# Kernel tuning notes

Hardware: AMD Instinct MI355X
Metric: run time of the kernel (lower is better)

Reference implementation:

```python
import jax, jax.numpy as jnp
import numpy as np

B, N, D = 2, 2048, 512
H, HD = 8, 64
R = 64  # graph_radius
SCALE = HD ** -0.5
LN_EPS = 1e-5


def _ln(x, g, b):
    m = jnp.mean(x, axis=-1, keepdims=True)
    v = jnp.mean((x - m) ** 2, axis=-1, keepdims=True)
    return (x - m) * jax.lax.rsqrt(v + LN_EPS) * g + b


def setup_inputs() -> dict:
    key = jax.random.key(0)
    ks = jax.random.split(key, 8)
    w = lambda k, shape: (jax.random.normal(k, shape, jnp.float32) * 0.02)
    return {
        "nodes": jax.random.normal(ks[0], (B, N, D), jnp.float32),
        "ln1_g": jnp.ones((D,), jnp.float32), "ln1_b": jnp.zeros((D,), jnp.float32),
        "qkv_w": w(ks[1], (D, 3 * D)), "qkv_b": jnp.zeros((3 * D,), jnp.float32),
        "proj_w": w(ks[2], (D, D)), "proj_b": jnp.zeros((D,), jnp.float32),
        "rep_scale": jnp.ones((H,), jnp.float32),
        "rel_bias": w(ks[3], (2 * N - 1, H)),
        "ln2_g": jnp.ones((D,), jnp.float32), "ln2_b": jnp.zeros((D,), jnp.float32),
        "mlp_w1": w(ks[4], (D, 2 * D)), "mlp_b1": jnp.zeros((2 * D,), jnp.float32),
        "mlp_w2": w(ks[5], (2 * D, D)), "mlp_b2": jnp.zeros((D,), jnp.float32),
    }


def reference(nodes, ln1_g, ln1_b, qkv_w, qkv_b, proj_w, proj_b, rep_scale,
              rel_bias, ln2_g, ln2_b, mlp_w1, mlp_b1, mlp_w2, mlp_b2):
    b, n, d = nodes.shape
    x = _ln(nodes, ln1_g, ln1_b)                       # [B,N,D]
    qkv = (x @ qkv_w + qkv_b).reshape(b, n, 3, H, HD)
    qkv = jnp.transpose(qkv, (2, 0, 3, 1, 4))          # [3,B,H,N,HD]
    q, k, v = qkv[0], qkv[1], qkv[2]
    logits = jnp.einsum('bhnd,bhmd->bhnm', q, k) * SCALE
    # representation correlation (F.normalize with eps=1e-12)
    rep = x / jnp.maximum(jnp.linalg.norm(x, axis=-1, keepdims=True), 1e-12)
    corr = jnp.einsum('bnd,bmd->bnm', rep, rep)        # [B,N,N]
    logits = logits + corr[:, None] * rep_scale[None, :, None, None]
    pos = jnp.arange(n)
    relidx = pos[:, None] - pos[None, :]               # [N,N]
    bias = rel_bias[relidx + n - 1]                    # [N,N,H]
    logits = logits + jnp.transpose(bias, (2, 0, 1))[None]
    mask = jnp.abs(relidx) <= R
    logits = jnp.where(mask[None, None], logits, -jnp.inf)
    attn = jax.nn.softmax(logits, axis=-1)
    upd = jnp.einsum('bhnm,bhmd->bnhd', attn, v).reshape(b, n, d)
    nodes = nodes + (upd @ proj_w + proj_b)
    y = _ln(nodes, ln2_g, ln2_b)
    h = jax.nn.gelu(y @ mlp_w1 + mlp_b1, approximate=False)
    return nodes + (h @ mlp_w2 + mlp_b2)
```

## Files before the change

### kernel.cpp

```cpp
#include <hip/hip_runtime.h>
#include <math.h>

typedef __bf16 bf16;
typedef __bf16 bf16x4 __attribute__((ext_vector_type(4)));
typedef __bf16 bf16x8 __attribute__((ext_vector_type(8)));
typedef float floatx4 __attribute__((ext_vector_type(4)));

#define BB 2
#define NN 2048
#define DD 512
#define HH 8
#define HD 64
#define RR 64
#define D3 1536
#define NEG_BIG (-1e30f)
#define TQ 32
#define TBAND 160

#define GL2LDS16(g, l)                                                        \
    __builtin_amdgcn_global_load_lds(                                         \
        (const __attribute__((address_space(1))) void*)(const void*)(g),      \
        (__attribute__((address_space(3))) void*)(void*)(l), 16, 0, 0)

static __device__ __forceinline__ float block_reduce_sum256(float v, float* sbuf) {
    const int tid = threadIdx.x;
    #pragma unroll
    for (int o = 32; o > 0; o >>= 1) v += __shfl_xor(v, o, 64);
    __syncthreads();
    if ((tid & 63) == 0) sbuf[tid >> 6] = v;
    __syncthreads();
    return sbuf[0] + sbuf[1] + sbuf[2] + sbuf[3];
}

static __device__ __forceinline__ void ln_row(
    float* sbuf, const float* in, const float* gw, const float* bw,
    bf16* out, float* invnorm, int row, bool want_inv) {
    const int tid = threadIdx.x;
    const int i0 = tid * 2;
    const float* ip = in + (size_t)row * DD;
    float v0 = ip[i0], v1 = ip[i0 + 1];
    float mean = block_reduce_sum256(v0 + v1, sbuf) * (1.f / DD);
    float d0 = v0 - mean, d1 = v1 - mean;
    float var = block_reduce_sum256(d0 * d0 + d1 * d1, sbuf) * (1.f / DD);
    float rs = rsqrtf(var + 1e-5f);
    float x0 = d0 * rs * gw[i0] + bw[i0];
    float x1 = d1 * rs * gw[i0 + 1] + bw[i0 + 1];
    out[(size_t)row * DD + i0] = (bf16)x0;
    out[(size_t)row * DD + i0 + 1] = (bf16)x1;
    if (want_inv) {
        float s2 = block_reduce_sum256(x0 * x0 + x1 * x1, sbuf);
        if (tid == 0) invnorm[row] = 1.f / fmaxf(sqrtf(s2), 1e-12f);
    }
}

union SMemCL {
    bf16 Ts[64][72];
    float sbuf[4];
};
__global__ __launch_bounds__(256) void cvt_ln_kernel(
    const float* __restrict__ qkv_w, const float* __restrict__ proj_w,
    const float* __restrict__ m1w, const float* __restrict__ m2w,
    bf16* __restrict__ wqt, bf16* __restrict__ wpt,
    bf16* __restrict__ w1t, bf16* __restrict__ w2t,
    const float* __restrict__ nodes, const float* __restrict__ ln1_g,
    const float* __restrict__ ln1_b, bf16* __restrict__ x,
    float* __restrict__ invn) {
    __shared__ SMemCL sm;
    const int tid = threadIdx.x;
    int bid = blockIdx.x;
    if (bid >= 512) {
        int r0 = (bid - 512) * 8;
        for (int r = 0; r < 8; r++)
            ln_row(sm.sbuf, nodes, ln1_g, ln1_b, x, invn, r0 + r, true);
        return;
    }
    const float* W; bf16* Wt; int K, N, bx, by;
    if (bid < 192)      { W = qkv_w; Wt = wqt; K = 512;  N = 1536; bx = bid % 24; by = bid / 24; }
    else if (bid < 256) { bid -= 192; W = proj_w; Wt = wpt; K = 512;  N = 512;  bx = bid % 8;  by = bid / 8; }
    else if (bid < 384) { bid -= 256; W = m1w; Wt = w1t; K = 512;  N = 1024; bx = bid % 16; by = bid / 16; }
    else                { bid -= 384; W = m2w; Wt = w2t; K = 1024; N = 512;  bx = bid % 8;  by = bid / 8; }
    const int n0 = bx * 64, k0 = by * 64;
    #pragma unroll
    for (int i = 0; i < 4; i++) {
        int r = (tid >> 4) + i * 16;
        int c = (tid & 15) * 4;
        floatx4 v = *(const floatx4*)(W + (size_t)(k0 + r) * N + n0 + c);
        #pragma unroll
        for (int e = 0; e < 4; e++) sm.Ts[r][c + e] = (bf16)v[e];
    }
    __syncthreads();
    #pragma unroll
    for (int i = 0; i < 4; i++) {
        int n = (tid >> 4) + i * 16;
        int k = (tid & 15) * 4;
        bf16x4 o;
        #pragma unroll
        for (int e = 0; e < 4; e++) o[e] = sm.Ts[k + e][n];
        *(bf16x4*)(Wt + (size_t)(n0 + n) * K + k0 + k) = o;
    }
}

union SMemQC {
    struct { bf16 As[2][4096], Bs[2][4096]; } g;
    struct { bf16 Ts[64][72]; } t;
    struct { bf16 Xc[TBAND * 72]; float invb[TBAND]; } c;
};
__global__ __launch_bounds__(256) void qkv_corr_kernel(
    const bf16* __restrict__ x, const bf16* __restrict__ wqt,
    const float* __restrict__ qkv_b, const float* __restrict__ invn,
    bf16* __restrict__ qkvb, bf16* __restrict__ vt_g,
    float* __restrict__ corr_g) {
    __shared__ SMemQC sm;
    const int tid = threadIdx.x;
    const int bid = blockIdx.x;
    const int w = tid >> 6, lane = tid & 63;
    const int lr = lane & 15, lq = lane >> 4;

    if (bid >= 1536) {
        const int item = bid - 1536;
        const int b = item & 1, n0 = (item >> 1) * TQ;
        const int bN = b * NN;
        const int rowHalf = (w >> 1) * 16, colBase = (w & 1) * 80;
        if (tid < TBAND) {
            int mc = min(max(n0 - RR + tid, 0), NN - 1);
            sm.c.invb[tid] = invn[bN + mc];
        }
        floatx4 cacc[5];
        #pragma unroll
        for (int t = 0; t < 5; t++) cacc[t] = (floatx4){0.f, 0.f, 0.f, 0.f};
        for (int c = 0; c < 8; c++) {
            __syncthreads();
            #pragma unroll
            for (int rr = 0; rr < 6; rr++) {
                int G = rr * 256 + tid;
                if (G < 1440) {
                    int j = G / 9, gc = G % 9;
                    int gcs = min(gc, 7);
                    int mc = min(max(n0 - RR + j, 0), NN - 1);
                    GL2LDS16(x + (size_t)(bN + mc) * DD + c * 64 + gcs * 8, sm.c.Xc + G * 8);
                }
            }
            __syncthreads();
            #pragma unroll
            for (int kb = 0; kb < 2; kb++) {
                bf16x8 a = *(bf16x8*)&sm.c.Xc[(64 + rowHalf + lr) * 72 + kb * 32 + lq * 8];
                #pragma unroll
                for (int t = 0; t < 5; t++) {
                    bf16x8 bb = *(bf16x8*)&sm.c.Xc[(colBase + t * 16 + lr) * 72 + kb * 32 + lq * 8];
                    cacc[t] = __builtin_amdgcn_mfma_f32_16x16x32_bf16(a, bb, cacc[t], 0, 0, 0);
                }
            }
        }
        float invq[4];
        #pragma unroll
        for (int r = 0; r < 4; r++) invq[r] = sm.c.invb[64 + rowHalf + lq * 4 + r];
        const size_t cbase = (size_t)item * TQ * TBAND;
        #pragma unroll
        for (int t = 0; t < 5; t++) {
            float invk = sm.c.invb[colBase + t * 16 + lr];
            #pragma unroll
            for (int r = 0; r < 4; r++)
                corr_g[cbase + (size_t)(rowHalf + lq * 4 + r) * TBAND + colBase + t * 16 + lr] =
                    cacc[t][r] * invq[r] * invk;
        }
        return;
    }

    const int bx = bid % 24, by = bid / 24;
    const int rowBase = by * 64, colBase = bx * 64;
    const int wm = (w >> 1) * 32, wn = (w & 1) * 32;

    floatx4 acc[2][2];
    #pragma unroll
    for (int i = 0; i < 2; i++)
        #pragma unroll
        for (int j = 0; j < 2; j++) acc[i][j] = (floatx4){0.f, 0.f, 0.f, 0.f};

    auto stage = [&](int buf, int k0) {
        #pragma unroll
        for (int i = 0; i < 2; i++) {
            int g = i * 256 + tid;
            int row = g >> 3, k8 = (g & 7) ^ (row & 7);
            GL2LDS16(x + (size_t)(rowBase + row) * DD + k0 + k8 * 8, &sm.g.As[buf][g * 8]);
        }
        #pragma unroll
        for (int i = 0; i < 2; i++) {
            int g = i * 256 + tid;
            int row = g >> 3, k8 = (g & 7) ^ (row & 7);
            GL2LDS16(wqt + (size_t)(colBase + row) * DD + k0 + k8 * 8, &sm.g.Bs[buf][g * 8]);
        }
    };

    stage(0, 0);
    for (int s = 0; s < 8; s++) {
        __syncthreads();
        if (s + 1 < 8) stage((s + 1) & 1, (s + 1) * 64);
        const int buf = s & 1;
        #pragma unroll
        for (int kb = 0; kb < 2; kb++) {
            bf16x8 af[2], bfr[2];
            #pragma unroll
            for (int i = 0; i < 2; i++) {
                int row = wm + i * 16 + lr;
                int g = row * 8 + ((kb * 4 + lq) ^ (row & 7));
                af[i] = *(bf16x8*)&sm.g.As[buf][g * 8];
            }
            #pragma unroll
            for (int j = 0; j < 2; j++) {
                int row = wn + j * 16 + lr;
                int g = row * 8 + ((kb * 4 + lq) ^ (row & 7));
                bfr[j] = *(bf16x8*)&sm.g.Bs[buf][g * 8];
            }
            #pragma unroll
            for (int i = 0; i < 2; i++)
                #pragma unroll
                for (int j = 0; j < 2; j++)
                    acc[i][j] = __builtin_amdgcn_mfma_f32_16x16x32_bf16(
                        af[i], bfr[j], acc[i][j], 0, 0, 0);
        }
    }

    if (bx < 16) {
        #pragma unroll
        for (int i = 0; i < 2; i++)
            #pragma unroll
            for (int j = 0; j < 2; j++)
                #pragma unroll
                for (int r = 0; r < 4; r++) {
                    int row = rowBase + wm + i * 16 + lq * 4 + r;
                    int col = colBase + wn + j * 16 + lr;
                    qkvb[(size_t)row * D3 + col] = (bf16)(acc[i][j][r] + qkv_b[col]);
                }
    } else {
        __syncthreads();
        #pragma unroll
        for (int i = 0; i < 2; i++)
            #pragma unroll
            for (int j = 0; j < 2; j++)
                #pragma unroll
                for (int r = 0; r < 4; r++) {
                    int nl = wm + i * 16 + lq * 4 + r;
                    int dl = wn + j * 16 + lr;
                    sm.t.Ts[nl][dl] = (bf16)(acc[i][j][r] + qkv_b[colBase + dl]);
                }
        __syncthreads();
        const int dV = colBase - 1024;
        #pragma unroll
        for (int i2 = 0; i2 < 2; i2++) {
            int d = (tid >> 3) + i2 * 32;
            int n8 = (tid & 7) * 8;
            bf16x8 o;
            #pragma unroll
            for (int e = 0; e < 8; e++) o[e] = sm.t.Ts[n8 + e][d];
            *(bf16x8*)(vt_g + (((size_t)(dV + d)) << 12) + rowBase + n8) = o;
        }
    }
}

template <int MODE>
__global__ __launch_bounds__(256) void gemm_bt(
    const bf16* __restrict__ A, const bf16* __restrict__ Bt,
    const float* __restrict__ bias, const float* __restrict__ resid,
    void* __restrict__ out, int M, int N, int K) {
    __shared__ __align__(16) bf16 As[2][64 * 64];
    __shared__ __align__(16) bf16 Bs[2][64 * 64];
    const int tid = threadIdx.x;
    const int w = tid >> 6, lane = tid & 63;
    const int lr = lane & 15, lq = lane >> 4;
    const int rowBase = blockIdx.y * 64, colBase = blockIdx.x * 64;
    const int wm = (w >> 1) * 32, wn = (w & 1) * 32;

    floatx4 acc[2][2];
    #pragma unroll
    for (int i = 0; i < 2; i++)
        #pragma unroll
        for (int j = 0; j < 2; j++) acc[i][j] = (floatx4){0.f, 0.f, 0.f, 0.f};

    auto stage = [&](int buf, int k0) {
        #pragma unroll
        for (int i = 0; i < 2; i++) {
            int g = i * 256 + tid;
            int row = g >> 3, k8 = (g & 7) ^ (row & 7);
            GL2LDS16(A + (size_t)(rowBase + row) * K + k0 + k8 * 8, &As[buf][g * 8]);
        }
        #pragma unroll
        for (int i = 0; i < 2; i++) {
            int g = i * 256 + tid;
            int row = g >> 3, k8 = (g & 7) ^ (row & 7);
            GL2LDS16(Bt + (size_t)(colBase + row) * K + k0 + k8 * 8, &Bs[buf][g * 8]);
        }
    };

    const int nsteps = K >> 6;
    stage(0, 0);
    for (int s = 0; s < nsteps; s++) {
        __syncthreads();
        if (s + 1 < nsteps) stage((s + 1) & 1, (s + 1) * 64);
        const int buf = s & 1;
        #pragma unroll
        for (int kb = 0; kb < 2; kb++) {
            bf16x8 af[2], bfr[2];
            #pragma unroll
            for (int i = 0; i < 2; i++) {
                int row = wm + i * 16 + lr;
                int g = row * 8 + ((kb * 4 + lq) ^ (row & 7));
                af[i] = *(bf16x8*)&As[buf][g * 8];
            }
            #pragma unroll
            for (int j = 0; j < 2; j++) {
                int row = wn + j * 16 + lr;
                int g = row * 8 + ((kb * 4 + lq) ^ (row & 7));
                bfr[j] = *(bf16x8*)&Bs[buf][g * 8];
            }
            #pragma unroll
            for (int i = 0; i < 2; i++)
                #pragma unroll
                for (int j = 0; j < 2; j++)
                    acc[i][j] = __builtin_amdgcn_mfma_f32_16x16x32_bf16(
                        af[i], bfr[j], acc[i][j], 0, 0, 0);
        }
    }

    #pragma unroll
    for (int i = 0; i < 2; i++) {
        #pragma unroll
        for (int j = 0; j < 2; j++) {
            #pragma unroll
            for (int r = 0; r < 4; r++) {
                int row = rowBase + wm + i * 16 + lq * 4 + r;
                int col = colBase + wn + j * 16 + lr;
                size_t idx = (size_t)row * N + col;
                float v = acc[i][j][r] + bias[col];
                if (MODE == 1) {
                    ((float*)out)[idx] = v + resid[idx];
                } else if (MODE == 2) {
                    float g = 0.5f * v * (1.f + erff(v * 0.70710678118654752f));
                    ((bf16*)out)[idx] = (bf16)g;
                } else {
                    ((float*)out)[idx] = v + resid[idx];
                }
            }
        }
    }
}

__global__ __launch_bounds__(256) void ln2_kernel(
    const float* __restrict__ in, const float* __restrict__ gw,
    const float* __restrict__ bw, bf16* __restrict__ out) {
    __shared__ float sbuf[4];
    ln_row(sbuf, in, gw, bw, out, nullptr, blockIdx.x, false);
}

__global__ __launch_bounds__(256) void attn_kernel(
    const bf16* __restrict__ qkv, const bf16* __restrict__ vt_g,
    const float* __restrict__ corr_g, const float* __restrict__ rep_scale,
    const float* __restrict__ rel_bias, bf16* __restrict__ upd) {
    __shared__ __align__(16) bf16 Qs[TQ * 136];
    __shared__ __align__(16) bf16 Ks[TBAND * 72];
    __shared__ __align__(16) bf16 Vt[64 * 168];
    __shared__ __align__(16) bf16 Ps[TQ * 168];
    __shared__ float relb[2][192];
    __shared__ float rmax2[TQ][2];
    __shared__ float rsum2[TQ][2];

    const int tid = threadIdx.x;
    const int item = blockIdx.x;
    const int b = item & 1;
    const int h0 = ((item >> 1) & 3) * 2;
    const int n0 = (item >> 3) * TQ;
    const int bN = b * NN;
    const int w = tid >> 6, lane = tid & 63;
    const int lr = lane & 15, lq = lane >> 4;
    const int rowHalf = (w >> 1) * 16;
    const int colBase = (w & 1) * 80;
    const int c2 = (w & 1) * 32;

    for (int idx = tid; idx < 2 * 191; idx += 256) {
        int hh = idx / 191, dh = idx - hh * 191;
        relb[hh][dh] = rel_bias[(size_t)(dh + (NN - 1 - 95)) * HH + h0 + hh];
    }

    float corrv[5][4];
    {
        const size_t cbase = (size_t)((((item >> 3)) << 1) | b) * TQ * TBAND;
        #pragma unroll
        for (int t = 0; t < 5; t++)
            #pragma unroll
            for (int r = 0; r < 4; r++)
                corrv[t][r] = corr_g[cbase + (size_t)(rowHalf + lq * 4 + r) * TBAND +
                                     colBase + t * 16 + lr];
    }

    #pragma unroll
    for (int rr = 0; rr < 3; rr++) {
        int G = rr * 256 + tid;
        if (G < 544) {
            int q = G / 17, gc = G % 17;
            int gcs = min(gc, 15);
            GL2LDS16(qkv + (size_t)(bN + n0 + q) * D3 + h0 * HD + gcs * 8, Qs + G * 8);
        }
    }

    for (int h = h0; h < h0 + 2; h++) {
        __syncthreads();
        #pragma unroll
        for (int rr = 0; rr < 6; rr++) {
            int G = rr * 256 + tid;
            if (G < 1440) {
                int j = G / 9, gc = G % 9;
                int gcs = min(gc, 7);
                int mc = min(max(n0 - RR + j, 0), NN - 1);
                GL2LDS16(qkv + (size_t)(bN + mc) * D3 + DD + h * HD + gcs * 8, Ks + G * 8);
            }
        }
        #pragma unroll
        for (int rr = 0; rr < 6; rr++) {
            int G = rr * 256 + tid;
            if (G < 1344) {
                int d = G / 21, gc = G % 21;
                int nsrc = min(max(n0 - RR + gc * 8, 0), NN - 8);
                GL2LDS16(vt_g + (((size_t)(h * HD + d)) << 12) + bN + nsrc, Vt + G * 8);
            }
        }
        __syncthreads();

        floatx4 sacc[5];
        #pragma unroll
        for (int t = 0; t < 5; t++) sacc[t] = (floatx4){0.f, 0.f, 0.f, 0.f};
        #pragma unroll
        for (int kb = 0; kb < 2; kb++) {
            bf16x8 a = *(bf16x8*)&Qs[(rowHalf + lr) * 136 + (h - h0) * 64 + kb * 32 + lq * 8];
            #pragma unroll
            for (int t = 0; t < 5; t++) {
                bf16x8 bb = *(bf16x8*)&Ks[(colBase + t * 16 + lr) * 72 + kb * 32 + lq * 8];
                sacc[t] = __builtin_amdgcn_mfma_f32_16x16x32_bf16(a, bb, sacc[t], 0, 0, 0);
            }
        }

        const float srep = rep_scale[h];
        float l[5][4];
        float mx[4] = {NEG_BIG, NEG_BIG, NEG_BIG, NEG_BIG};
        #pragma unroll
        for (int t = 0; t < 5; t++) {
            int j = colBase + t * 16 + lr;
            int m = n0 - RR + j;
            #pragma unroll
            for (int r = 0; r < 4; r++) {
                int qi = rowHalf + lq * 4 + r;
                int relidx = qi + RR - j;
                bool valid = (relidx >= -RR) && (relidx <= RR) && (m >= 0) && (m < NN);
                float lv = sacc[t][r] * 0.125f + corrv[t][r] * srep +
                           relb[h - h0][relidx + 95];
                l[t][r] = valid ? lv : NEG_BIG;
                mx[r] = fmaxf(mx[r], l[t][r]);
            }
        }
        #pragma unroll
        for (int r = 0; r < 4; r++)
            #pragma unroll
            for (int mk = 1; mk <= 8; mk <<= 1)
                mx[r] = fmaxf(mx[r], __shfl_xor(mx[r], mk, 64));
        if (lr == 0) {
            #pragma unroll
            for (int r = 0; r < 4; r++) rmax2[rowHalf + lq * 4 + r][w & 1] = mx[r];
        }
        __syncthreads();

        float rm[4], sme[4];
        #pragma unroll
        for (int r = 0; r < 4; r++) {
            int row = rowHalf + lq * 4 + r;
            rm[r] = fmaxf(rmax2[row][0], rmax2[row][1]);
            sme[r] = 0.f;
        }
        #pragma unroll
        for (int t = 0; t < 5; t++) {
            int j = colBase + t * 16 + lr;
            #pragma unroll
            for (int r = 0; r < 4; r++) {
                float pv = __expf(l[t][r] - rm[r]);
                sme[r] += pv;
                Ps[(rowHalf + lq * 4 + r) * 168 + j] = (bf16)pv;
            }
        }
        #pragma unroll
        for (int r = 0; r < 4; r++)
            #pragma unroll
            for (int mk = 1; mk <= 8; mk <<= 1)
                sme[r] += __shfl_xor(sme[r], mk, 64);
        if (lr == 0) {
            #pragma unroll
            for (int r = 0; r < 4; r++) rsum2[rowHalf + lq * 4 + r][w & 1] = sme[r];
        }
        __syncthreads();

        floatx4 oacc[2] = {(floatx4){0.f, 0.f, 0.f, 0.f}, (floatx4){0.f, 0.f, 0.f, 0.f}};
        #pragma unroll
        for (int kb = 0; kb < 5; kb++) {
            bf16x8 a = *(bf16x8*)&Ps[(rowHalf + lr) * 168 + kb * 32 + lq * 8];
            #pragma unroll
            for (int tt = 0; tt < 2; tt++) {
                bf16x8 bb = *(bf16x8*)&Vt[(c2 + tt * 16 + lr) * 168 + kb * 32 + lq * 8];
                oacc[tt] = __builtin_amdgcn_mfma_f32_16x16x32_bf16(a, bb, oacc[tt], 0, 0, 0);
            }
        }
        #pragma unroll
        for (int r = 0; r < 4; r++) {
            int row = rowHalf + lq * 4 + r;
            float rinv = 1.f / (rsum2[row][0] + rsum2[row][1]);
            #pragma unroll
            for (int tt = 0; tt < 2; tt++) {
                upd[(size_t)(bN + n0 + row) * DD + h * HD + c2 + tt * 16 + lr] =
                    (bf16)(oacc[tt][r] * rinv);
            }
        }
    }
}

extern "C" void kernel_launch(void* const* d_in, const int* in_sizes, int n_in,
                              void* d_out, int out_size, void* d_ws,
                              size_t ws_size, hipStream_t stream) {
    const float* nodes  = (const float*)d_in[0];
    const float* ln1_g  = (const float*)d_in[1];
    const float* ln1_b  = (const float*)d_in[2];
    const float* qkv_w  = (const float*)d_in[3];
    const float* qkv_b  = (const float*)d_in[4];
    const float* proj_w = (const float*)d_in[5];
    const float* proj_b = (const float*)d_in[6];
    const float* rep_s  = (const float*)d_in[7];
    const float* rel_b  = (const float*)d_in[8];
    const float* ln2_g  = (const float*)d_in[9];
    const float* ln2_b  = (const float*)d_in[10];
    const float* mlp_w1 = (const float*)d_in[11];
    const float* mlp_b1 = (const float*)d_in[12];
    const float* mlp_w2 = (const float*)d_in[13];
    const float* mlp_b2 = (const float*)d_in[14];

    char* p = (char*)d_ws;
    float* invn = (float*)p;            p += (size_t)1 << 20;
    bf16*  wqt  = (bf16*)p;             p += (size_t)DD * D3 * 2;
    bf16*  wpt  = (bf16*)p;             p += (size_t)DD * DD * 2;
    bf16*  w1t  = (bf16*)p;             p += (size_t)DD * 2 * DD * 2;
    bf16*  w2t  = (bf16*)p;             p += (size_t)2 * DD * DD * 2;
    bf16*  x    = (bf16*)p;             p += (size_t)BB * NN * DD * 2;
    bf16*  qkvb = (bf16*)p;             p += (size_t)BB * NN * D3 * 2;
    char*  regA = p;                    p += (size_t)BB * NN * DD * 4;
    float* corr_g = (float*)regA;
    bf16*  vt_g   = (bf16*)(regA + (size_t)BB * (NN / TQ) * TQ * TBAND * 4);
    float* mid    = (float*)regA;
    bf16*  y    = x;
    bf16*  hgl  = qkvb;
    bf16*  upd  = (bf16*)d_out;

    const int M = BB * NN;

    cvt_ln_kernel<<<1024, 256, 0, stream>>>(
        qkv_w, proj_w, mlp_w1, mlp_w2, wqt, wpt, w1t, w2t,
        nodes, ln1_g, ln1_b, x, invn);
    qkv_corr_kernel<<<1664, 256, 0, stream>>>(
        x, wqt, qkv_b, invn, qkvb, vt_g, corr_g);
    attn_kernel<<<512, 256, 0, stream>>>(
        qkvb, vt_g, corr_g, rep_s, rel_b, upd);
    gemm_bt<1><<<dim3(DD / 64, M / 64), 256, 0, stream>>>(
        upd, wpt, proj_b, nodes, mid, M, DD, DD);
    ln2_kernel<<<M, 256, 0, stream>>>(mid, ln2_g, ln2_b, y);
    gemm_bt<2><<<dim3(2 * DD / 64, M / 64), 256, 0, stream>>>(
        y, w1t, mlp_b1, nullptr, hgl, M, 2 * DD, DD);
    gemm_bt<3><<<dim3(DD / 64, M / 64), 256, 0, stream>>>(
        hgl, w2t, mlp_b2, mid, (float*)d_out, M, DD, 2 * DD);
}
```

Before: 185.7 us.

## Switch GEMMs to 128x128 single-buffered tiles and split V transpose out

```diff
diff --git a/kernel.cpp b/kernel.cpp
--- a/kernel.cpp
+++ b/kernel.cpp
@@ -100,24 +100,114 @@
     }
 }
 
+template <int MODE>
+static __device__ __forceinline__ void gemm128_body(
+    bf16* As, bf16* Bs, const bf16* A, const bf16* Bt,
+    const float* bias, const float* resid, void* out,
+    int N, int K, int bx, int by) {
+    const int tid = threadIdx.x;
+    const int w = tid >> 6, lane = tid & 63;
+    const int lr = lane & 15, lq = lane >> 4;
+    const int rowBase = by * 128, colBase = bx * 128;
+    const int wm = (w >> 1) * 64, wn = (w & 1) * 64;
+
+    floatx4 acc[4][4];
+    #pragma unroll
+    for (int i = 0; i < 4; i++)
+        #pragma unroll
+        for (int j = 0; j < 4; j++) acc[i][j] = (floatx4){0.f, 0.f, 0.f, 0.f};
+
+    for (int k0 = 0; k0 < K; k0 += 64) {
+        __syncthreads();
+        #pragma unroll
+        for (int i = 0; i < 4; i++) {
+            int g = i * 256 + tid;
+            int row = g >> 3, k8 = (g & 7) ^ (row & 7);
+            GL2LDS16(A + (size_t)(rowBase + row) * K + k0 + k8 * 8, As + g * 8);
+        }
+        #pragma unroll
+        for (int i = 0; i < 4; i++) {
+            int g = i * 256 + tid;
+            int row = g >> 3, k8 = (g & 7) ^ (row & 7);
+            GL2LDS16(Bt + (size_t)(colBase + row) * K + k0 + k8 * 8, Bs + g * 8);
+        }
+        __syncthreads();
+        #pragma unroll
+        for (int kb = 0; kb < 2; kb++) {
+            bf16x8 af[4], bfr[4];
+            #pragma unroll
+            for (int i = 0; i < 4; i++) {
+                int row = wm + i * 16 + lr;
+                int g = row * 8 + ((kb * 4 + lq) ^ (row & 7));
+                af[i] = *(bf16x8*)&As[g * 8];
+            }
+            #pragma unroll
+            for (int j = 0; j < 4; j++) {
+                int row = wn + j * 16 + lr;
+                int g = row * 8 + ((kb * 4 + lq) ^ (row & 7));
+                bfr[j] = *(bf16x8*)&Bs[g * 8];
+            }
+            #pragma unroll
+            for (int i = 0; i < 4; i++)
+                #pragma unroll
+                for (int j = 0; j < 4; j++)
+                    acc[i][j] = __builtin_amdgcn_mfma_f32_16x16x32_bf16(
+                        af[i], bfr[j], acc[i][j], 0, 0, 0);
+        }
+    }
+
+    #pragma unroll
+    for (int i = 0; i < 4; i++) {
+        #pragma unroll
+        for (int j = 0; j < 4; j++) {
+            #pragma unroll
+            for (int r = 0; r < 4; r++) {
+                int row = rowBase + wm + i * 16 + lq * 4 + r;
+                int col = colBase + wn + j * 16 + lr;
+                size_t idx = (size_t)row * N + col;
+                float v = acc[i][j][r] + bias[col];
+                if (MODE == 0) {
+                    ((bf16*)out)[idx] = (bf16)v;
+                } else if (MODE == 1) {
+                    ((float*)out)[idx] = v + resid[idx];
+                } else if (MODE == 2) {
+                    float g = 0.5f * v * (1.f + erff(v * 0.70710678118654752f));
+                    ((bf16*)out)[idx] = (bf16)g;
+                } else {
+                    ((float*)out)[idx] = v + resid[idx];
+                }
+            }
+        }
+    }
+}
+
+template <int MODE>
+__global__ __launch_bounds__(256) void gemm128_kernel(
+    const bf16* __restrict__ A, const bf16* __restrict__ Bt,
+    const float* __restrict__ bias, const float* __restrict__ resid,
+    void* __restrict__ out, int N, int K) {
+    __shared__ __align__(16) bf16 As[128 * 64];
+    __shared__ __align__(16) bf16 Bs[128 * 64];
+    gemm128_body<MODE>(As, Bs, A, Bt, bias, resid, out, N, K,
+                       blockIdx.x, blockIdx.y);
+}
+
 union SMemQC {
-    struct { bf16 As[2][4096], Bs[2][4096]; } g;
-    struct { bf16 Ts[64][72]; } t;
+    struct { bf16 As[128 * 64], Bs[128 * 64]; } g;
     struct { bf16 Xc[TBAND * 72]; float invb[TBAND]; } c;
 };
 __global__ __launch_bounds__(256) void qkv_corr_kernel(
     const bf16* __restrict__ x, const bf16* __restrict__ wqt,
     const float* __restrict__ qkv_b, const float* __restrict__ invn,
-    bf16* __restrict__ qkvb, bf16* __restrict__ vt_g,
-    float* __restrict__ corr_g) {
+    bf16* __restrict__ qkvb, float* __restrict__ corr_g) {
     __shared__ SMemQC sm;
     const int tid = threadIdx.x;
     const int bid = blockIdx.x;
     const int w = tid >> 6, lane = tid & 63;
     const int lr = lane & 15, lq = lane >> 4;
 
-    if (bid >= 1536) {
-        const int item = bid - 1536;
+    if (bid < 128) {
+        const int item = bid;
         const int b = item & 1, n0 = (item >> 1) * TQ;
         const int bN = b * NN;
         const int rowHalf = (w >> 1) * 16, colBase = (w & 1) * 80;
@@ -166,181 +256,31 @@
         return;
     }
 
-    const int bx = bid % 24, by = bid / 24;
-    const int rowBase = by * 64, colBase = bx * 64;
-    const int wm = (w >> 1) * 32, wn = (w & 1) * 32;
-
-    floatx4 acc[2][2];
-    #pragma unroll
-    for (int i = 0; i < 2; i++)
-        #pragma unroll
-        for (int j = 0; j < 2; j++) acc[i][j] = (floatx4){0.f, 0.f, 0.f, 0.f};
-
-    auto stage = [&](int buf, int k0) {
-        #pragma unroll
-        for (int i = 0; i < 2; i++) {
-            int g = i * 256 + tid;
-            int row = g >> 3, k8 = (g & 7) ^ (row & 7);
-            GL2LDS16(x + (size_t)(rowBase + row) * DD + k0 + k8 * 8, &sm.g.As[buf][g * 8]);
-        }
-        #pragma unroll
-        for (int i = 0; i < 2; i++) {
-            int g = i * 256 + tid;
-            int row = g >> 3, k8 = (g & 7) ^ (row & 7);
-            GL2LDS16(wqt + (size_t)(colBase + row) * DD + k0 + k8 * 8, &sm.g.Bs[buf][g * 8]);
-        }
-    };
-
-    stage(0, 0);
-    for (int s = 0; s < 8; s++) {
-        __syncthreads();
-        if (s + 1 < 8) stage((s + 1) & 1, (s + 1) * 64);
-        const int buf = s & 1;
-        #pragma unroll
-        for (int kb = 0; kb < 2; kb++) {
-            bf16x8 af[2], bfr[2];
-            #pragma unroll
-            for (int i = 0; i < 2; i++) {
-                int row = wm + i * 16 + lr;
-                int g = row * 8 + ((kb * 4 + lq) ^ (row & 7));
-                af[i] = *(bf16x8*)&sm.g.As[buf][g * 8];
-            }
-            #pragma unroll
-            for (int j = 0; j < 2; j++) {
-                int row = wn + j * 16 + lr;
-                int g = row * 8 + ((kb * 4 + lq) ^ (row & 7));
-                bfr[j] = *(bf16x8*)&sm.g.Bs[buf][g * 8];
-            }
-            #pragma unroll
-            for (int i = 0; i < 2; i++)
-                #pragma unroll
-                for (int j = 0; j < 2; j++)
-                    acc[i][j] = __builtin_amdgcn_mfma_f32_16x16x32_bf16(
-                        af[i], bfr[j], acc[i][j], 0, 0, 0);
-        }
-    }
-
-    if (bx < 16) {
-        #pragma unroll
-        for (int i = 0; i < 2; i++)
-            #pragma unroll
-            for (int j = 0; j < 2; j++)
-                #pragma unroll
-                for (int r = 0; r < 4; r++) {
-                    int row = rowBase + wm + i * 16 + lq * 4 + r;
-                    int col = colBase + wn + j * 16 + lr;
-                    qkvb[(size_t)row * D3 + col] = (bf16)(acc[i][j][r] + qkv_b[col]);
-                }
-    } else {
-        __syncthreads();
-        #pragma unroll
-        for (int i = 0; i < 2; i++)
-            #pragma unroll
-            for (int j = 0; j < 2; j++)
-                #pragma unroll
-                for (int r = 0; r < 4; r++) {
-                    int nl = wm + i * 16 + lq * 4 + r;
-                    int dl = wn + j * 16 + lr;
-                    sm.t.Ts[nl][dl] = (bf16)(acc[i][j][r] + qkv_b[colBase + dl]);
-                }
-        __syncthreads();
-        const int dV = colBase - 1024;
-        #pragma unroll
-        for (int i2 = 0; i2 < 2; i2++) {
-            int d = (tid >> 3) + i2 * 32;
-            int n8 = (tid & 7) * 8;
-            bf16x8 o;
-            #pragma unroll
-            for (int e = 0; e < 8; e++) o[e] = sm.t.Ts[n8 + e][d];
-            *(bf16x8*)(vt_g + (((size_t)(dV + d)) << 12) + rowBase + n8) = o;
-        }
-    }
-}
-
-template <int MODE>
-__global__ __launch_bounds__(256) void gemm_bt(
-    const bf16* __restrict__ A, const bf16* __restrict__ Bt,
-    const float* __restrict__ bias, const float* __restrict__ resid,
-    void* __restrict__ out, int M, int N, int K) {
-    __shared__ __align__(16) bf16 As[2][64 * 64];
-    __shared__ __align__(16) bf16 Bs[2][64 * 64];
-    const int tid = threadIdx.x;
-    const int w = tid >> 6, lane = tid & 63;
-    const int lr = lane & 15, lq = lane >> 4;
-    const int rowBase = blockIdx.y * 64, colBase = blockIdx.x * 64;
-    const int wm = (w >> 1) * 32, wn = (w & 1) * 32;
-
-    floatx4 acc[2][2];
-    #pragma unroll
-    for (int i = 0; i < 2; i++)
-        #pragma unroll
-        for (int j = 0; j < 2; j++) acc[i][j] = (floatx4){0.f, 0.f, 0.f, 0.f};
-
-    auto stage = [&](int buf, int k0) {
-        #pragma unroll
-        for (int i = 0; i < 2; i++) {
-            int g = i * 256 + tid;
-            int row = g >> 3, k8 = (g & 7) ^ (row & 7);
-            GL2LDS16(A + (size_t)(rowBase + row) * K + k0 + k8 * 8, &As[buf][g * 8]);
-        }
-        #pragma unroll
-        for (int i = 0; i < 2; i++) {
-            int g = i * 256 + tid;
-            int row = g >> 3, k8 = (g & 7) ^ (row & 7);
-            GL2LDS16(Bt + (size_t)(colBase + row) * K + k0 + k8 * 8, &Bs[buf][g * 8]);
-        }
-    };
-
-    const int nsteps = K >> 6;
-    stage(0, 0);
-    for (int s = 0; s < nsteps; s++) {
-        __syncthreads();
-        if (s + 1 < nsteps) stage((s + 1) & 1, (s + 1) * 64);
-        const int buf = s & 1;
-        #pragma unroll
-        for (int kb = 0; kb < 2; kb++) {
-            bf16x8 af[2], bfr[2];
-            #pragma unroll
-            for (int i = 0; i < 2; i++) {
-                int row = wm + i * 16 + lr;
-                int g = row * 8 + ((kb * 4 + lq) ^ (row & 7));
-                af[i] = *(bf16x8*)&As[buf][g * 8];
-            }
-            #pragma unroll
-            for (int j = 0; j < 2; j++) {
-                int row = wn + j * 16 + lr;
-                int g = row * 8 + ((kb * 4 + lq) ^ (row & 7));
-                bfr[j] = *(bf16x8*)&Bs[buf][g * 8];
-            }
-            #pragma unroll
-            for (int i = 0; i < 2; i++)
-                #pragma unroll
-                for (int j = 0; j < 2; j++)
-                    acc[i][j] = __builtin_amdgcn_mfma_f32_16x16x32_bf16(
-                        af[i], bfr[j], acc[i][j], 0, 0, 0);
-        }
-    }
-
+    const int idx = bid - 128;
+    gemm128_body<0>(sm.g.As, sm.g.Bs, x, wqt, qkv_b, nullptr, qkvb,
+                    D3, DD, idx % 12, idx / 12);
+}
+
+__global__ __launch_bounds__(256) void vtrans_kernel(
+    const bf16* __restrict__ qkvb, bf16* __restrict__ vt_g) {
+    __shared__ bf16 Ts[64][72];
+    const int tid = threadIdx.x;
+    const int r0 = blockIdx.x * 64;
+    const int h = blockIdx.y;
     #pragma unroll
     for (int i = 0; i < 2; i++) {
-        #pragma unroll
-        for (int j = 0; j < 2; j++) {
-            #pragma unroll
-            for (int r = 0; r < 4; r++) {
-                int row = rowBase + wm + i * 16 + lq * 4 + r;
-                int col = colBase + wn + j * 16 + lr;
-                size_t idx = (size_t)row * N + col;
-                float v = acc[i][j][r] + bias[col];
-                if (MODE == 1) {
-                    ((float*)out)[idx] = v + resid[idx];
-                } else if (MODE == 2) {
-                    float g = 0.5f * v * (1.f + erff(v * 0.70710678118654752f));
-                    ((bf16*)out)[idx] = (bf16)g;
-                } else {
-                    ((float*)out)[idx] = v + resid[idx];
-                }
-            }
-        }
+        int r = (tid >> 3) + i * 32, c8 = tid & 7;
+        *(bf16x8*)&Ts[r][c8 * 8] =
+            *(const bf16x8*)(qkvb + (size_t)(r0 + r) * D3 + 2 * DD + h * HD + c8 * 8);
+    }
+    __syncthreads();
+    #pragma unroll
+    for (int i = 0; i < 2; i++) {
+        int d = (tid >> 3) + i * 32, c8 = (tid & 7) * 8;
+        bf16x8 o;
+        #pragma unroll
+        for (int e = 0; e < 8; e++) o[e] = Ts[c8 + e][d];
+        *(bf16x8*)(vt_g + (((size_t)(h * HD + d)) << 12) + r0 + c8) = o;
     }
 }
 
@@ -557,15 +497,16 @@
     cvt_ln_kernel<<<1024, 256, 0, stream>>>(
         qkv_w, proj_w, mlp_w1, mlp_w2, wqt, wpt, w1t, w2t,
         nodes, ln1_g, ln1_b, x, invn);
-    qkv_corr_kernel<<<1664, 256, 0, stream>>>(
-        x, wqt, qkv_b, invn, qkvb, vt_g, corr_g);
+    qkv_corr_kernel<<<512, 256, 0, stream>>>(
+        x, wqt, qkv_b, invn, qkvb, corr_g);
+    vtrans_kernel<<<dim3(M / 64, HH), 256, 0, stream>>>(qkvb, vt_g);
     attn_kernel<<<512, 256, 0, stream>>>(
         qkvb, vt_g, corr_g, rep_s, rel_b, upd);
-    gemm_bt<1><<<dim3(DD / 64, M / 64), 256, 0, stream>>>(
-        upd, wpt, proj_b, nodes, mid, M, DD, DD);
+    gemm128_kernel<1><<<dim3(DD / 128, M / 128), 256, 0, stream>>>(
+        upd, wpt, proj_b, nodes, mid, DD, DD);
     ln2_kernel<<<M, 256, 0, stream>>>(mid, ln2_g, ln2_b, y);
-    gemm_bt<2><<<dim3(2 * DD / 64, M / 64), 256, 0, stream>>>(
-        y, w1t, mlp_b1, nullptr, hgl, M, 2 * DD, DD);
-    gemm_bt<3><<<dim3(DD / 64, M / 64), 256, 0, stream>>>(
-        hgl, w2t, mlp_b2, mid, (float*)d_out, M, DD, 2 * DD);
-}
+    gemm128_kernel<2><<<dim3(2 * DD / 128, M / 128), 256, 0, stream>>>(
+        y, w1t, mlp_b1, nullptr, hgl, 2 * DD, DD);
+    gemm128_kernel<3><<<dim3(DD / 128, M / 128), 256, 0, stream>>>(
+        hgl, w2t, mlp_b2, mid, (float*)d_out, DD, 2 * DD);
+}
```

New measurement: 190.4 us. 2.5% more time.
